# Performance work log

Measured on AMD Instinct MI355X. Metric: run time of the kernel, lower is better.

Reference implementation:

```python
import jax, jax.numpy as jnp
import numpy as np

B, N, C = 4, 2048, 1024
H = 16
HD = C // H
SCALE = HD ** -0.5


def setup_inputs() -> dict:
    key = jax.random.key(0)
    ks = jax.random.split(key, 5)
    s = 0.02
    return {
        "x": jax.random.normal(ks[0], (B, N, C), dtype=jnp.float32),
        "w_qkv": jax.random.normal(ks[1], (C, 3 * C), dtype=jnp.float32) * s,
        "b_qkv": jnp.zeros((3 * C,), dtype=jnp.float32),
        "w_proj": jax.random.normal(ks[2], (C, C), dtype=jnp.float32) * s,
        "b_proj": jnp.zeros((C,), dtype=jnp.float32),
    }


def reference(x, w_qkv, b_qkv, w_proj, b_proj):
    b, n, c = x.shape
    qkv = x @ w_qkv + b_qkv                       # [b, n, 3c]
    qkv = qkv.reshape(b, n, 3, H, HD)
    qkv = jnp.transpose(qkv, (2, 0, 3, 1, 4))     # [3, b, h, n, hd]
    q, k, v = qkv[0], qkv[1], qkv[2]
    attn = jnp.einsum("bhqd,bhkd->bhqk", q, k) * SCALE
    attn = jax.nn.softmax(attn, axis=-1)
    out = jnp.einsum("bhqk,bhkd->bhqd", attn, v)  # [b, h, n, hd]
    out = jnp.transpose(out, (0, 2, 1, 3)).reshape(b, n, c)
    return out @ w_proj + b_proj
```

## Files before the change

### kernel.cpp

```cpp
#include <hip/hip_runtime.h>
#include <cstdint>
#include <cstddef>


typedef __attribute__((ext_vector_type(8))) short short8;
typedef __attribute__((ext_vector_type(4))) float f32x4;

#if __has_builtin(__builtin_amdgcn_exp2f)
#define EXP2F(x) __builtin_amdgcn_exp2f(x)
#else
#define EXP2F(x) __expf((x) * 0.69314718056f)
#endif

__device__ __forceinline__ short f2bf(float x) {
  unsigned u = __builtin_bit_cast(unsigned, x);
  u += 0x7fffu + ((u >> 16) & 1u);
  return (short)(u >> 16);
}

__device__ __forceinline__ void async16(const void* g, void* l) {
  __builtin_amdgcn_global_load_lds(
      (const __attribute__((address_space(1))) unsigned*)g,
      (__attribute__((address_space(3))) unsigned*)l, 16, 0, 0);
}


__global__ __launch_bounds__(256) void convert_kernel(const float* __restrict__ in,
                                                      short* __restrict__ out) {
  int i = blockIdx.x * 256 + threadIdx.x;
  const float4* p = (const float4*)in + (size_t)i * 2;
  float4 a = p[0], b = p[1];
  short8 r;
  r[0] = f2bf(a.x); r[1] = f2bf(a.y); r[2] = f2bf(a.z); r[3] = f2bf(a.w);
  r[4] = f2bf(b.x); r[5] = f2bf(b.y); r[6] = f2bf(b.z); r[7] = f2bf(b.w);
  *((short8*)out + i) = r;
}

__global__ __launch_bounds__(256) void wtrans_kernel(const float* __restrict__ in,
                                                     short* __restrict__ out,
                                                     int K, int N) {
  __shared__ float tile[32][33];
  int n0 = blockIdx.x * 32, k0 = blockIdx.y * 32;
  int tx = threadIdx.x, ty = threadIdx.y;
  for (int r = ty; r < 32; r += 8)
    tile[r][tx] = in[(size_t)(k0 + r) * N + n0 + tx];
  __syncthreads();
  for (int r = ty; r < 32; r += 8)
    out[(size_t)(n0 + r) * K + k0 + tx] = f2bf(tile[tx][r]);
}


template <int MODE>
__global__ __launch_bounds__(256) void gemm_kernel(
    const short* __restrict__ A, const short* __restrict__ Bt,
    const float* __restrict__ bias, int Nn,
    short* __restrict__ qb, short* __restrict__ kb, short* __restrict__ vtb,
    float* __restrict__ outp) {
  constexpr int K = 1024;
  __shared__ __align__(16) short As[128 * 32];
  __shared__ __align__(16) short Bs[128 * 32];
  const int tid = threadIdx.x, wave = tid >> 6, lane = tid & 63;
  const int quad = lane >> 4, l16 = lane & 15;
  const int m0 = blockIdx.y * 128, n0 = blockIdx.x * 128;
  const int wrow = (wave >> 1) * 64, wcol = (wave & 1) * 64;

  const int str = lane >> 2;
  const int sgc = ((lane & 3) ^ ((lane >> 3) & 3)) * 8;
  const short* Ag = A + (size_t)(m0 + str) * K + sgc;
  const short* Bg = Bt + (size_t)(n0 + str) * K + sgc;

  const int fsw = (l16 >> 1) & 3;

  f32x4 acc[4][4] = {};

  for (int k0 = 0; k0 < K; k0 += 32) {
#pragma unroll
    for (int i = 0; i < 2; ++i) {
      int c = wave * 2 + i;
      async16(Ag + (size_t)c * 16 * K + k0, (char*)As + c * 1024);
      async16(Bg + (size_t)c * 16 * K + k0, (char*)Bs + c * 1024);
    }
    __syncthreads();
    short8 af[4], bf[4];
#pragma unroll
    for (int t = 0; t < 4; ++t) {
      af[t] = *(const short8*)&As[(wrow + t * 16 + l16) * 32 + ((quad ^ fsw) << 3)];
      bf[t] = *(const short8*)&Bs[(wcol + t * 16 + l16) * 32 + ((quad ^ fsw) << 3)];
    }
#pragma unroll
    for (int mt = 0; mt < 4; ++mt)
#pragma unroll
      for (int nt = 0; nt < 4; ++nt)
        acc[mt][nt] = __builtin_amdgcn_mfma_f32_16x16x32_bf16(af[mt], bf[nt],
                                                              acc[mt][nt], 0, 0, 0);
    __syncthreads();
  }

  if (MODE == 0) {
#pragma unroll
    for (int mt = 0; mt < 4; ++mt) {
      int row0 = m0 + wrow + mt * 16 + quad * 4;
      int b = row0 >> 11, n = row0 & 2047;
#pragma unroll
      for (int nt = 0; nt < 4; ++nt) {
        int col = n0 + wcol + nt * 16 + l16;
        float bv = bias[col];
        float v0 = acc[mt][nt][0] + bv, v1 = acc[mt][nt][1] + bv;
        float v2 = acc[mt][nt][2] + bv, v3 = acc[mt][nt][3] + bv;
        int which = col >> 10;
        int h = (col >> 6) & 15;
        int d = col & 63;
        size_t bh = (size_t)(b * 16 + h);
        if (which == 0) {
          const float qs = 0.18033688f;
          size_t base = (bh * 2048 + n) * 64 + d;
          qb[base]       = f2bf(v0 * qs);
          qb[base + 64]  = f2bf(v1 * qs);
          qb[base + 128] = f2bf(v2 * qs);
          qb[base + 192] = f2bf(v3 * qs);
        } else if (which == 1) {
          size_t base = (bh * 2048 + n) * 64 + d;
          kb[base]       = f2bf(v0);
          kb[base + 64]  = f2bf(v1);
          kb[base + 128] = f2bf(v2);
          kb[base + 192] = f2bf(v3);
        } else {
          ushort4 pk;
          pk.x = (unsigned short)f2bf(v0);
          pk.y = (unsigned short)f2bf(v1);
          pk.z = (unsigned short)f2bf(v2);
          pk.w = (unsigned short)f2bf(v3);
          *(ushort4*)&vtb[(bh * 64 + d) * 2048 + n] = pk;
        }
      }
    }
  } else {
#pragma unroll
    for (int mt = 0; mt < 4; ++mt) {
      int row0 = m0 + wrow + mt * 16 + quad * 4;
#pragma unroll
      for (int nt = 0; nt < 4; ++nt) {
        int col = n0 + wcol + nt * 16 + l16;
        float bv = bias[col];
        outp[(size_t)row0 * Nn + col]       = acc[mt][nt][0] + bv;
        outp[(size_t)(row0 + 1) * Nn + col] = acc[mt][nt][1] + bv;
        outp[(size_t)(row0 + 2) * Nn + col] = acc[mt][nt][2] + bv;
        outp[(size_t)(row0 + 3) * Nn + col] = acc[mt][nt][3] + bv;
      }
    }
  }
}


__global__ __launch_bounds__(256) void attn_kernel(
    const short* __restrict__ qb, const short* __restrict__ kb,
    const short* __restrict__ vtb, short* __restrict__ ob) {
  __shared__ __align__(16) short Ks[64 * 64];
  __shared__ __align__(16) short Vs[64 * 64];
  __shared__ __align__(16) short Ps[4][32 * 64];
  __shared__ __align__(16) float Ls[4][32];
  const int tid = threadIdx.x, wave = tid >> 6, lane = tid & 63;
  const int quad = lane >> 4, l16 = lane & 15;
  const int q0 = blockIdx.x * 128;
  const int bh = blockIdx.y;
  const short* Qg = qb + (size_t)bh * (2048 * 64);
  const short* Kg = kb + (size_t)bh * (2048 * 64);
  const short* Vg = vtb + (size_t)bh * (64 * 2048);

  short8 qf[2][2];
#pragma unroll
  for (int qt = 0; qt < 2; ++qt)
#pragma unroll
    for (int kc = 0; kc < 2; ++kc)
      qf[qt][kc] = *(const short8*)
          &Qg[(size_t)(q0 + wave * 32 + qt * 16 + l16) * 64 + kc * 32 + quad * 8];

  const int str = lane >> 3;
  const int sgc = ((lane & 7) ^ (str & 7)) * 8;
  const int fsw = l16 & 7;
  short* Pw = Ps[wave];

  float lsum[2] = {0.f, 0.f};
  f32x4 oacc[2][4] = {};

  for (int kv0 = 0; kv0 < 2048; kv0 += 64) {
#pragma unroll
    for (int i = 0; i < 2; ++i) {
      int c = wave * 2 + i;
      async16(Kg + (size_t)(kv0 + c * 8 + str) * 64 + sgc, (char*)Ks + c * 1024);
      async16(Vg + (size_t)(c * 8 + str) * 2048 + kv0 + sgc, (char*)Vs + c * 1024);
    }
    __syncthreads();

    f32x4 sacc[2][4] = {};
#pragma unroll
    for (int kc = 0; kc < 2; ++kc) {
      short8 kf[4];
#pragma unroll
      for (int kvt = 0; kvt < 4; ++kvt)
        kf[kvt] = *(const short8*)
            &Ks[(kvt * 16 + l16) * 64 + (((kc * 4 + quad) ^ fsw) << 3)];
#pragma unroll
      for (int kvt = 0; kvt < 4; ++kvt)
#pragma unroll
        for (int qt = 0; qt < 2; ++qt)
          sacc[qt][kvt] = __builtin_amdgcn_mfma_f32_16x16x32_bf16(
              kf[kvt], qf[qt][kc], sacc[qt][kvt], 0, 0, 0);
    }

#pragma unroll
    for (int qt = 0; qt < 2; ++qt)
#pragma unroll
      for (int kvt = 0; kvt < 4; ++kvt) {
        float p0 = EXP2F(sacc[qt][kvt][0]);
        float p1 = EXP2F(sacc[qt][kvt][1]);
        float p2 = EXP2F(sacc[qt][kvt][2]);
        float p3 = EXP2F(sacc[qt][kvt][3]);
        lsum[qt] += (p0 + p1) + (p2 + p3);
        unsigned u0 = __builtin_bit_cast(unsigned, p0) + 0x8000u;
        unsigned u1 = __builtin_bit_cast(unsigned, p1) + 0x8000u;
        unsigned u2 = __builtin_bit_cast(unsigned, p2) + 0x8000u;
        unsigned u3 = __builtin_bit_cast(unsigned, p3) + 0x8000u;
        uint2 w;
        w.x = (u0 >> 16) | (u1 & 0xffff0000u);
        w.y = (u2 >> 16) | (u3 & 0xffff0000u);
        *(uint2*)&Pw[(qt * 16 + l16) * 64 +
                     ((((kvt * 2 + (quad >> 1)) ^ fsw)) << 3) + (quad & 1) * 4] = w;
      }

    __asm__ volatile("s_waitcnt lgkmcnt(0)" ::: "memory");

#pragma unroll
    for (int kc = 0; kc < 2; ++kc) {
      short8 pf[2], vf[4];
#pragma unroll
      for (int qt = 0; qt < 2; ++qt)
        pf[qt] = *(const short8*)
            &Pw[(qt * 16 + l16) * 64 + (((kc * 4 + quad) ^ fsw) << 3)];
#pragma unroll
      for (int nt = 0; nt < 4; ++nt)
        vf[nt] = *(const short8*)
            &Vs[(nt * 16 + l16) * 64 + (((kc * 4 + quad) ^ fsw) << 3)];
#pragma unroll
      for (int qt = 0; qt < 2; ++qt)
#pragma unroll
        for (int nt = 0; nt < 4; ++nt)
          oacc[qt][nt] = __builtin_amdgcn_mfma_f32_16x16x32_bf16(
              pf[qt], vf[nt], oacc[qt][nt], 0, 0, 0);
    }
    __syncthreads();
  }

#pragma unroll
  for (int qt = 0; qt < 2; ++qt) {
    float v = lsum[qt];
    v += __shfl_xor(v, 16, 64);
    v += __shfl_xor(v, 32, 64);
    if (quad == 0) Ls[wave][qt * 16 + l16] = v;
  }
  __asm__ volatile("s_waitcnt lgkmcnt(0)" ::: "memory");

  const int b = bh >> 4, h = bh & 15;
#pragma unroll
  for (int qt = 0; qt < 2; ++qt) {
    float4 lr = *(const float4*)&Ls[wave][qt * 16 + quad * 4];
    float inv0 = 1.f / lr.x, inv1 = 1.f / lr.y, inv2 = 1.f / lr.z, inv3 = 1.f / lr.w;
#pragma unroll
    for (int nt = 0; nt < 4; ++nt) {
      int d = nt * 16 + l16;
      int qbase = q0 + wave * 32 + qt * 16 + quad * 4;
      size_t obase = ((size_t)(b * 2048 + qbase)) * 1024 + h * 64 + d;
      ob[obase]        = f2bf(oacc[qt][nt][0] * inv0);
      ob[obase + 1024] = f2bf(oacc[qt][nt][1] * inv1);
      ob[obase + 2048] = f2bf(oacc[qt][nt][2] * inv2);
      ob[obase + 3072] = f2bf(oacc[qt][nt][3] * inv3);
    }
  }
}


extern "C" void kernel_launch(void* const* d_in, const int* in_sizes, int n_in,
                              void* d_out, int out_size, void* d_ws, size_t ws_size,
                              hipStream_t stream) {
  const float* x      = (const float*)d_in[0];
  const float* w_qkv  = (const float*)d_in[1];
  const float* b_qkv  = (const float*)d_in[2];
  const float* w_proj = (const float*)d_in[3];
  const float* b_proj = (const float*)d_in[4];
  float* out = (float*)d_out;

  short* xs     = (short*)d_ws;
  short* wqkvT  = xs + (size_t)8192 * 1024;
  short* wprojT = wqkvT + (size_t)3072 * 1024;
  short* qb     = wprojT + (size_t)1024 * 1024;
  short* kb     = qb + (size_t)64 * 2048 * 64;
  short* vtb    = kb + (size_t)64 * 2048 * 64;
  short* aob    = vtb + (size_t)64 * 2048 * 64;

  convert_kernel<<<dim3(4096), 256, 0, stream>>>(x, xs);
  wtrans_kernel<<<dim3(96, 32), dim3(32, 8), 0, stream>>>(w_qkv, wqkvT, 1024, 3072);
  wtrans_kernel<<<dim3(32, 32), dim3(32, 8), 0, stream>>>(w_proj, wprojT, 1024, 1024);

  gemm_kernel<0><<<dim3(24, 64), 256, 0, stream>>>(xs, wqkvT, b_qkv, 3072,
                                                   qb, kb, vtb, nullptr);
  attn_kernel<<<dim3(16, 64), 256, 0, stream>>>(qb, kb, vtb, aob);
  gemm_kernel<1><<<dim3(8, 64), 256, 0, stream>>>(aob, wprojT, b_proj, 1024,
                                                  nullptr, nullptr, nullptr, out);
}
```

Before: 303.4 us.

## Double-buffer K/V tiles in attention to overlap loads with compute

Allocates two shared-memory buffers each for K and V. It prefetches the first tile before the loop, then issues the async global-to-LDS loads for tile t+1 right after the barrier at the top of iteration t. The tile loads now run during the QK^T, softmax and PV work of the current tile, and the trailing barrier in each iteration goes away. In exchange it doubles K/V shared memory, which can lower occupancy, and it relies on the top barrier waiting for the outstanding async loads.

Measured after the change: 307.1 us. No clear change (+1.2%).

```diff
diff --git a/kernel.cpp b/kernel.cpp
--- a/kernel.cpp
+++ b/kernel.cpp
@@ -155,8 +155,8 @@
 __global__ __launch_bounds__(256) void attn_kernel(
     const short* __restrict__ qb, const short* __restrict__ kb,
     const short* __restrict__ vtb, short* __restrict__ ob) {
-  __shared__ __align__(16) short Ks[64 * 64];
-  __shared__ __align__(16) short Vs[64 * 64];
+  __shared__ __align__(16) short Ks[2][64 * 64];
+  __shared__ __align__(16) short Vs[2][64 * 64];
   __shared__ __align__(16) short Ps[4][32 * 64];
   __shared__ __align__(16) float Ls[4][32];
   const int tid = threadIdx.x, wave = tid >> 6, lane = tid & 63;
@@ -179,18 +179,31 @@
   const int sgc = ((lane & 7) ^ (str & 7)) * 8;
   const int fsw = l16 & 7;
   short* Pw = Ps[wave];
+  const int c0 = wave * 2, c1 = wave * 2 + 1;
+
+  async16(Kg + (size_t)(c0 * 8 + str) * 64 + sgc, (char*)Ks[0] + c0 * 1024);
+  async16(Kg + (size_t)(c1 * 8 + str) * 64 + sgc, (char*)Ks[0] + c1 * 1024);
+  async16(Vg + (size_t)(c0 * 8 + str) * 2048 + sgc, (char*)Vs[0] + c0 * 1024);
+  async16(Vg + (size_t)(c1 * 8 + str) * 2048 + sgc, (char*)Vs[0] + c1 * 1024);
 
   float lsum[2] = {0.f, 0.f};
   f32x4 oacc[2][4] = {};
 
-  for (int kv0 = 0; kv0 < 2048; kv0 += 64) {
-#pragma unroll
-    for (int i = 0; i < 2; ++i) {
-      int c = wave * 2 + i;
-      async16(Kg + (size_t)(kv0 + c * 8 + str) * 64 + sgc, (char*)Ks + c * 1024);
-      async16(Vg + (size_t)(c * 8 + str) * 2048 + kv0 + sgc, (char*)Vs + c * 1024);
-    }
+#pragma unroll 2
+  for (int t = 0; t < 32; ++t) {
     __syncthreads();
+
+    int kvn = (t + 1) * 64;
+    if (kvn < 2048) {
+      char* kd = (char*)Ks[(t + 1) & 1];
+      char* vd = (char*)Vs[(t + 1) & 1];
+      async16(Kg + (size_t)(kvn + c0 * 8 + str) * 64 + sgc, kd + c0 * 1024);
+      async16(Kg + (size_t)(kvn + c1 * 8 + str) * 64 + sgc, kd + c1 * 1024);
+      async16(Vg + (size_t)(c0 * 8 + str) * 2048 + kvn + sgc, vd + c0 * 1024);
+      async16(Vg + (size_t)(c1 * 8 + str) * 2048 + kvn + sgc, vd + c1 * 1024);
+    }
+    const short* Kst = Ks[t & 1];
+    const short* Vst = Vs[t & 1];
 
     f32x4 sacc[2][4] = {};
 #pragma unroll
@@ -199,7 +212,7 @@
 #pragma unroll
       for (int kvt = 0; kvt < 4; ++kvt)
         kf[kvt] = *(const short8*)
-            &Ks[(kvt * 16 + l16) * 64 + (((kc * 4 + quad) ^ fsw) << 3)];
+            &Kst[(kvt * 16 + l16) * 64 + (((kc * 4 + quad) ^ fsw) << 3)];
 #pragma unroll
       for (int kvt = 0; kvt < 4; ++kvt)
 #pragma unroll
@@ -240,7 +253,7 @@
 #pragma unroll
       for (int nt = 0; nt < 4; ++nt)
         vf[nt] = *(const short8*)
-            &Vs[(nt * 16 + l16) * 64 + (((kc * 4 + quad) ^ fsw) << 3)];
+            &Vst[(nt * 16 + l16) * 64 + (((kc * 4 + quad) ^ fsw) << 3)];
 #pragma unroll
       for (int qt = 0; qt < 2; ++qt)
 #pragma unroll
@@ -248,7 +261,6 @@
           oacc[qt][nt] = __builtin_amdgcn_mfma_f32_16x16x32_bf16(
               pf[qt], vf[nt], oacc[qt][nt], 0, 0, 0);
     }
-    __syncthreads();
   }
 
 #pragma unroll
```
